# Kernel tuning notes

Measured on AMD Instinct MI355X. Metric: run time of the kernel, lower is better.

The kernel has to match this reference:

```python
import jax, jax.numpy as jnp
import numpy as np
import math

C = 256
GROUPS = 32
EPS = 1e-5

def setup_inputs() -> dict:
    key = jax.random.key(0)
    ks = jax.random.split(key, 11)
    B, H, W = 8, 64, 64
    s = 1.0 / math.sqrt(C)
    return {
        "x": jax.random.normal(ks[0], (B, C, H, W), dtype=jnp.float32),
        "gamma": jnp.ones((C,), jnp.float32),
        "beta": jnp.zeros((C,), jnp.float32),
        "wq": jax.random.normal(ks[1], (C, C), jnp.float32) * s,
        "bq": jnp.zeros((C,), jnp.float32),
        "wk": jax.random.normal(ks[2], (C, C), jnp.float32) * s,
        "bk": jnp.zeros((C,), jnp.float32),
        "wv": jax.random.normal(ks[3], (C, C), jnp.float32) * s,
        "bv": jnp.zeros((C,), jnp.float32),
        "wp": jax.random.normal(ks[4], (C, C), jnp.float32) * s,
        "bp": jnp.zeros((C,), jnp.float32),
    }

def _group_norm(x, gamma, beta):
    B, Cc, H, W = x.shape
    xg = x.reshape(B, GROUPS, Cc // GROUPS, H, W)
    mu = xg.mean(axis=(2, 3, 4), keepdims=True)
    var = xg.var(axis=(2, 3, 4), keepdims=True)
    xn = ((xg - mu) * jax.lax.rsqrt(var + EPS)).reshape(B, Cc, H, W)
    return xn * gamma[None, :, None, None] + beta[None, :, None, None]

def reference(x, gamma, beta, wq, bq, wk, bk, wv, bv, wp, bp):
    B, Cc, H, W = x.shape
    T = H * W
    h = _group_norm(x, gamma, beta)           # (B,C,H,W)
    hf = h.reshape(B, Cc, T)                  # (B,C,T)
    # 1x1 convs = per-pixel linear maps over channels
    q = jnp.einsum('oc,bct->bto', wq, hf) + bq           # (B,T,C)
    k = jnp.einsum('oc,bct->bot', wk, hf) + bk[:, None]  # (B,C,T)
    v = jnp.einsum('oc,bct->bto', wv, hf) + bv           # (B,T,C)
    scores = jnp.einsum('btc,bcs->bts', q, k) / math.sqrt(Cc)
    attn = jax.nn.softmax(scores, axis=-1)    # (B,T,T)
    z = jnp.einsum('bts,bsc->btc', attn, v)   # (B,T,C)
    zf = z.transpose(0, 2, 1)                 # (B,C,T)
    proj = jnp.einsum('oc,bct->bot', wp, zf) + bp[:, None]
    return x + proj.reshape(B, Cc, H, W)
```

## Files before the change

### kernel.cpp

```cpp
#include <hip/hip_runtime.h>


typedef unsigned short u16;
typedef unsigned char u8;
typedef __attribute__((ext_vector_type(8))) short short8;
typedef __attribute__((ext_vector_type(4))) float f32x4;

#define MFMA16(a, b, c) __builtin_amdgcn_mfma_f32_16x16x32_bf16((a), (b), (c), 0, 0, 0)
#define MFMA16F8(a, b, c) __builtin_amdgcn_mfma_f32_16x16x32_fp8_fp8((a), (b), (c), 0, 0, 0)

#define GLL16(g, l)                                                            \
  __builtin_amdgcn_global_load_lds(                                            \
      (const __attribute__((address_space(1))) void*)(g),                      \
      (__attribute__((address_space(3))) void*)(l), 16, 0, 0)

#define BAR_VM8()  asm volatile("s_waitcnt vmcnt(8)\n\ts_barrier" ::: "memory")
#define BAR_VM4()  asm volatile("s_waitcnt vmcnt(4)\n\ts_barrier" ::: "memory")
#define BAR_LGKM() asm volatile("s_waitcnt lgkmcnt(0)\n\ts_barrier" ::: "memory")

#define CVT_PK_BF16(dst, lo, hi)                                               \
  asm("v_cvt_pk_bf16_f32 %0, %1, %2" : "=v"(dst) : "v"(lo), "v"(hi))

__device__ __forceinline__ u16 f2bf(float f) {
  union { float f; unsigned u; } v; v.f = f;
  unsigned u = v.u;
  return (u16)((u + 0x7FFFu + ((u >> 16) & 1u)) >> 16);
}

__device__ __forceinline__ u8 f2fp8(float f) {
  int p = __builtin_amdgcn_cvt_pk_fp8_f32(f, f, 0, false);
  return (u8)(p & 0xff);
}

__global__ __launch_bounds__(256) void prep(
    const float* __restrict__ x,
    const float* __restrict__ gamma, const float* __restrict__ beta,
    const float* __restrict__ wq, const float* __restrict__ wk,
    const float* __restrict__ wv, const float* __restrict__ wp,
    u16* __restrict__ wb, u16* __restrict__ h_t) {
  const int bid = blockIdx.x, tid = threadIdx.x;
  if (bid < 256) {
    const int m = bid >> 6;
    const float* s = (m == 0) ? wq : (m == 1) ? wk : (m == 2) ? wv : wp;
    const int i = ((bid & 63) * 256 + tid) * 4;
    float4 v = *(const float4*)(s + i);
    u16* d = wb + m * 65536 + i;
    d[0] = f2bf(v.x); d[1] = f2bf(v.y); d[2] = f2bf(v.z); d[3] = f2bf(v.w);
    return;
  }
  const int gid = bid - 256;
  const int b = gid >> 5, g = gid & 31;
  const float* p = x + (long)gid * 32768;

  float s = 0.f, ss = 0.f;
  #pragma unroll 8
  for (int i = 0; i < 32; ++i) {
    float4 v = *(const float4*)(p + tid * 4 + i * 1024);
    s  += v.x + v.y + v.z + v.w;
    ss += v.x * v.x + v.y * v.y + v.z * v.z + v.w * v.w;
  }
  for (int off = 32; off; off >>= 1) {
    s  += __shfl_down(s, off);
    ss += __shfl_down(ss, off);
  }
  __shared__ float2 red[4];
  __shared__ float2 stat;
  if ((tid & 63) == 0) red[tid >> 6] = make_float2(s, ss);
  __syncthreads();
  if (tid == 0) {
    float S  = red[0].x + red[1].x + red[2].x + red[3].x;
    float SS = red[0].y + red[1].y + red[2].y + red[3].y;
    float mean = S * (1.f / 32768.f);
    float var  = SS * (1.f / 32768.f) - mean * mean;
    stat = make_float2(mean, rsqrtf(var + 1e-5f));
  }
  __syncthreads();
  const float mean = stat.x, rstd = stat.y;

  __shared__ float tile[8][257];
  const int cr = tid >> 5;
  const int c_g = g * 8;
  const float gm = gamma[c_g + cr] * rstd;
  const float bt = beta[c_g + cr] - mean * gm;
  const float* xc = x + ((long)(b * 256 + c_g + cr) * 4096);
  u16* hb = h_t + ((long)b * 4096) * 256 + c_g;

  for (int ch = 0; ch < 16; ++ch) {
    const int t0 = ch * 256;
    {
      const int tj = (tid & 31) * 8;
      float4 v0 = *(const float4*)(xc + t0 + tj);
      float4 v1 = *(const float4*)(xc + t0 + tj + 4);
      tile[cr][tj + 0] = v0.x * gm + bt;
      tile[cr][tj + 1] = v0.y * gm + bt;
      tile[cr][tj + 2] = v0.z * gm + bt;
      tile[cr][tj + 3] = v0.w * gm + bt;
      tile[cr][tj + 4] = v1.x * gm + bt;
      tile[cr][tj + 5] = v1.y * gm + bt;
      tile[cr][tj + 6] = v1.z * gm + bt;
      tile[cr][tj + 7] = v1.w * gm + bt;
    }
    __syncthreads();
    {
      uint4 o;
      CVT_PK_BF16(o.x, tile[0][tid], tile[1][tid]);
      CVT_PK_BF16(o.y, tile[2][tid], tile[3][tid]);
      CVT_PK_BF16(o.z, tile[4][tid], tile[5][tid]);
      CVT_PK_BF16(o.w, tile[6][tid], tile[7][tid]);
      *(uint4*)(hb + (long)(t0 + tid) * 256) = o;
    }
    __syncthreads();
  }
}

template <bool ROW_BIAS, bool RESID>
__global__ __launch_bounds__(256, 2) void gemm_bt(
    const u16* __restrict__ A, long strideAz, const u16* __restrict__ B,
    long strideBz, const float* __restrict__ bias, float scale,
    u16* __restrict__ outb, float* __restrict__ outf,
    const float* __restrict__ resid, long strideOz, int N) {
  __shared__ u16 a_lds[128 * 32];
  __shared__ u16 b_lds[128 * 32];
  const int tid = threadIdx.x, w = tid >> 6, l = tid & 63;
  const int l15 = l & 15, l4 = l >> 4;
  const int bz = blockIdx.z;
  A += bz * strideAz;
  B += bz * strideBz;
  const long obase = (long)bz * strideOz;
  const int m0 = blockIdx.y * 128, n0 = blockIdx.x * 128;
  const int wm = (w >> 1) * 64, wn = (w & 1) * 64;

  f32x4 acc[4][4];
  #pragma unroll
  for (int i = 0; i < 4; ++i)
    #pragma unroll
    for (int j = 0; j < 4; ++j) acc[i][j] = (f32x4)0.f;

  for (int kt = 0; kt < 8; ++kt) {
    const int k0 = kt * 32;
    __syncthreads();
    #pragma unroll
    for (int j = 0; j < 2; ++j) {
      const int r0 = (w * 2 + j) * 16;
      const int row = r0 + (l >> 2);
      const int sg = (l & 3) ^ (row & 3);
      GLL16(A + (long)(m0 + row) * 256 + k0 + sg * 8, a_lds + r0 * 32);
      GLL16(B + (long)(n0 + row) * 256 + k0 + sg * 8, b_lds + r0 * 32);
    }
    __syncthreads();
    short8 af[4], bf[4];
    #pragma unroll
    for (int t = 0; t < 4; ++t) {
      const int ra = wm + t * 16 + l15;
      af[t] = *(const short8*)(a_lds + ra * 32 + ((l4 ^ (ra & 3)) * 8));
      const int rb = wn + t * 16 + l15;
      bf[t] = *(const short8*)(b_lds + rb * 32 + ((l4 ^ (rb & 3)) * 8));
    }
    #pragma unroll
    for (int mt = 0; mt < 4; ++mt)
      #pragma unroll
      for (int nt = 0; nt < 4; ++nt) acc[mt][nt] = MFMA16(af[mt], bf[nt], acc[mt][nt]);
  }

  if (!ROW_BIAS) {
    float bv[4];
    #pragma unroll
    for (int nt = 0; nt < 4; ++nt) bv[nt] = bias[n0 + wn + nt * 16 + l15];
    #pragma unroll
    for (int mt = 0; mt < 4; ++mt)
      #pragma unroll
      for (int nt = 0; nt < 4; ++nt)
        #pragma unroll
        for (int r = 0; r < 4; ++r) {
          const int row = m0 + wm + mt * 16 + l4 * 4 + r;
          const int col = n0 + wn + nt * 16 + l15;
          outb[obase + (long)row * N + col] = f2bf((acc[mt][nt][r] + bv[nt]) * scale);
        }
  } else {
    float bm[4][4];
    #pragma unroll
    for (int mt = 0; mt < 4; ++mt)
      #pragma unroll
      for (int r = 0; r < 4; ++r) bm[mt][r] = bias[m0 + wm + mt * 16 + l4 * 4 + r];
    #pragma unroll
    for (int mt = 0; mt < 4; ++mt)
      #pragma unroll
      for (int nt = 0; nt < 4; ++nt)
        #pragma unroll
        for (int r = 0; r < 4; ++r) {
          const int row = m0 + wm + mt * 16 + l4 * 4 + r;
          const int col = n0 + wn + nt * 16 + l15;
          const long idx = obase + (long)row * N + col;
          float v = acc[mt][nt][r] + bm[mt][r];
          if (RESID) outf[idx] = v + resid[idx];
          else       outb[idx] = f2bf(v);
        }
  }
}

__global__ __launch_bounds__(256, 2) void gemm_qk(
    const u16* __restrict__ A, const u16* __restrict__ Bw,
    const float* __restrict__ bq, const float* __restrict__ bk,
    u8* __restrict__ Qs8, u8* __restrict__ Ks8) {
  __shared__ u16 a_lds[128 * 32];
  __shared__ u16 b_lds[128 * 32];
  const int tid = threadIdx.x, w = tid >> 6, l = tid & 63;
  const int l15 = l & 15, l4 = l >> 4;
  const int m0 = blockIdx.y * 128, n0 = blockIdx.x * 128;
  const int wm = (w >> 1) * 64, wn = (w & 1) * 64;

  f32x4 acc[4][4];
  #pragma unroll
  for (int i = 0; i < 4; ++i)
    #pragma unroll
    for (int j = 0; j < 4; ++j) acc[i][j] = (f32x4)0.f;

  for (int kt = 0; kt < 8; ++kt) {
    const int k0 = kt * 32;
    __syncthreads();
    #pragma unroll
    for (int j = 0; j < 2; ++j) {
      const int r0 = (w * 2 + j) * 16;
      const int row = r0 + (l >> 2);
      const int sg = (l & 3) ^ (row & 3);
      GLL16(A + (long)(m0 + row) * 256 + k0 + sg * 8, a_lds + r0 * 32);
      GLL16(Bw + (long)(n0 + row) * 256 + k0 + sg * 8, b_lds + r0 * 32);
    }
    __syncthreads();
    short8 af[4], bf[4];
    #pragma unroll
    for (int t = 0; t < 4; ++t) {
      const int ra = wm + t * 16 + l15;
      af[t] = *(const short8*)(a_lds + ra * 32 + ((l4 ^ (ra & 3)) * 8));
      const int rb = wn + t * 16 + l15;
      bf[t] = *(const short8*)(b_lds + rb * 32 + ((l4 ^ (rb & 3)) * 8));
    }
    #pragma unroll
    for (int mt = 0; mt < 4; ++mt)
      #pragma unroll
      for (int nt = 0; nt < 4; ++nt) acc[mt][nt] = MFMA16(af[mt], bf[nt], acc[mt][nt]);
  }

  const bool isQ = n0 < 256;
  u8* out = isQ ? Qs8 : Ks8;
  const float* bias = isQ ? bq : bk;
  const float osc = isQ ? 0.25f : 0.36067376022224085f;
  const int nc0 = n0 & 255;
  float bv[4];
  #pragma unroll
  for (int nt = 0; nt < 4; ++nt) bv[nt] = bias[nc0 + wn + nt * 16 + l15];
  #pragma unroll
  for (int mt = 0; mt < 4; ++mt)
    #pragma unroll
    for (int nt = 0; nt < 4; ++nt)
      #pragma unroll
      for (int r = 0; r < 4; ++r) {
        const int row = m0 + wm + mt * 16 + l4 * 4 + r;
        const int col = nc0 + wn + nt * 16 + l15;
        out[(long)row * 256 + col] = f2fp8((acc[mt][nt][r] + bv[nt]) * osc);
      }
}

__global__ __launch_bounds__(256, 2) void attn_kernel(
    const u8* __restrict__ Qs8, const u8* __restrict__ Ks8,
    const u16* __restrict__ Vt, u16* __restrict__ Z) {
  __shared__ u8  k_lds8[16384];
  __shared__ u16 v_lds[16384];
  __shared__ u16 p_lds[64 * 72];
  __shared__ float l_red[256];

  const int tid = threadIdx.x, w = tid >> 6, l = tid & 63;
  const int l15 = l & 15, l4 = l >> 4;
  const int bid = blockIdx.x;
  const int batch = bid & 7;
  const int qt = bid >> 3;
  const int ws0 = (w & 1) * 32, wq0 = (w >> 1) * 32, wcolO = (w & 1) * 128;
  const long qrow_base = (long)batch * 4096 + qt * 64;

  const u8*  kbase = Ks8 + (long)batch * 4096 * 256;
  const u16* vbase = Vt + (long)batch * 256 * 4096;

  long qf[2][8];
  {
    const u8* qp = Qs8 + (qrow_base + wq0) * 256;
    #pragma unroll
    for (int qt2 = 0; qt2 < 2; ++qt2)
      #pragma unroll
      for (int ks = 0; ks < 8; ++ks)
        qf[qt2][ks] = *(const long*)(qp + (qt2 * 16 + l15) * 256 + ks * 32 + l4 * 8);
  }

  const int cvv = 8 * w + (l >> 3);
  const int sgv = (l & 7) ^ (cvv & 7);

  f32x4 o_acc[2][8];
  #pragma unroll
  for (int mt = 0; mt < 2; ++mt)
    #pragma unroll
    for (int nt = 0; nt < 8; ++nt) o_acc[mt][nt] = (f32x4)0.f;
  float rs2[2] = {0.f, 0.f};

  #pragma unroll
  for (int j = 0; j < 4; ++j) {
    const int r0 = (j * 4 + w) * 4;
    const int row = r0 + (l >> 4);
    const int g = (l & 15) ^ (row & 15);
    GLL16(kbase + (long)row * 256 + g * 16, k_lds8 + r0 * 256);
  }
  #pragma unroll
  for (int j = 0; j < 8; ++j) {
    const int c0 = (j * 4 + w) * 8;
    GLL16(vbase + (long)(c0 + (l >> 3)) * 4096 + sgv * 8, v_lds + c0 * 64);
  }

  for (int st = 0; st < 64; ++st) {
    const int snn = ((st + 1) & 63) * 64;

    BAR_VM8();

    f32x4 sacc[2][2];
    #pragma unroll
    for (int i = 0; i < 2; ++i)
      #pragma unroll
      for (int j = 0; j < 2; ++j) sacc[i][j] = (f32x4)0.f;
    __builtin_amdgcn_s_setprio(1);
    #pragma unroll
    for (int ks = 0; ks < 8; ++ks) {
      long kf[2];
      #pragma unroll
      for (int st2 = 0; st2 < 2; ++st2) {
        const int row = ws0 + st2 * 16 + l15;
        const int g = (ks * 2 + (l4 >> 1)) ^ l15;
        kf[st2] = *(const long*)(k_lds8 + row * 256 + g * 16 + (l4 & 1) * 8);
      }
      #pragma unroll
      for (int st2 = 0; st2 < 2; ++st2)
        #pragma unroll
        for (int qt2 = 0; qt2 < 2; ++qt2)
          sacc[st2][qt2] = MFMA16F8(kf[st2], qf[qt2][ks], sacc[st2][qt2]);
    }
    __builtin_amdgcn_s_setprio(0);

    #pragma unroll
    for (int st2 = 0; st2 < 2; ++st2)
      #pragma unroll
      for (int qt2 = 0; qt2 < 2; ++qt2) {
        float e0 = __builtin_exp2f(sacc[st2][qt2][0]);
        float e1 = __builtin_exp2f(sacc[st2][qt2][1]);
        float e2 = __builtin_exp2f(sacc[st2][qt2][2]);
        float e3 = __builtin_exp2f(sacc[st2][qt2][3]);
        rs2[qt2] += (e0 + e1) + (e2 + e3);
        unsigned pw0, pw1;
        CVT_PK_BF16(pw0, e0, e1);
        CVT_PK_BF16(pw1, e2, e3);
        *(uint2*)(p_lds + (wq0 + qt2 * 16 + l15) * 72 + ws0 + st2 * 16 + l4 * 4) =
            make_uint2(pw0, pw1);
      }

    BAR_LGKM();

    #pragma unroll
    for (int j = 0; j < 4; ++j) {
      const int r0 = (j * 4 + w) * 4;
      const int row = r0 + (l >> 4);
      const int g = (l & 15) ^ (row & 15);
      GLL16(kbase + (long)(snn + row) * 256 + g * 16, k_lds8 + r0 * 256);
    }

    BAR_VM4();

    __builtin_amdgcn_s_setprio(1);
    #pragma unroll
    for (int ks2 = 0; ks2 < 2; ++ks2) {
      short8 pa[2];
      #pragma unroll
      for (int mt = 0; mt < 2; ++mt)
        pa[mt] = *(const short8*)(p_lds + (wq0 + mt * 16 + l15) * 72 + ks2 * 32 + l4 * 8);
      #pragma unroll
      for (int nt = 0; nt < 8; ++nt) {
        const int c = wcolO + nt * 16 + l15;
        const int gv = (ks2 * 4 + l4) ^ (c & 7);
        short8 vb = *(const short8*)(v_lds + c * 64 + gv * 8);
        #pragma unroll
        for (int mt = 0; mt < 2; ++mt) o_acc[mt][nt] = MFMA16(pa[mt], vb, o_acc[mt][nt]);
      }
    }
    __builtin_amdgcn_s_setprio(0);

    BAR_LGKM();

    #pragma unroll
    for (int j = 0; j < 8; ++j) {
      const int c0 = (j * 4 + w) * 8;
      GLL16(vbase + (long)(c0 + (l >> 3)) * 4096 + snn + sgv * 8, v_lds + c0 * 64);
    }
  }

  #pragma unroll
  for (int qt2 = 0; qt2 < 2; ++qt2) {
    float v = rs2[qt2];
    v += __shfl_xor(v, 16);
    v += __shfl_xor(v, 32);
    if (l4 == 0) l_red[w * 64 + wq0 + qt2 * 16 + l15] = v;
  }
  __syncthreads();
  if (tid < 64) {
    const int w0 = (tid >> 5) * 2;
    float t = l_red[w0 * 64 + tid] + l_red[(w0 + 1) * 64 + tid];
    l_red[tid] = 1.f / t;
  }
  __syncthreads();

  #pragma unroll
  for (int mt = 0; mt < 2; ++mt) {
    float inv[4];
    #pragma unroll
    for (int r = 0; r < 4; ++r) inv[r] = l_red[wq0 + mt * 16 + l4 * 4 + r];
    #pragma unroll
    for (int nt = 0; nt < 8; ++nt) {
      const int col = wcolO + nt * 16 + l15;
      #pragma unroll
      for (int r = 0; r < 4; ++r) {
        const long row = qrow_base + wq0 + mt * 16 + l4 * 4 + r;
        Z[row * 256 + col] = f2bf(o_acc[mt][nt][r] * inv[r]);
      }
    }
  }
}

extern "C" void kernel_launch(void* const* d_in, const int* in_sizes, int n_in,
                              void* d_out, int out_size, void* d_ws, size_t ws_size,
                              hipStream_t stream) {
  (void)in_sizes; (void)n_in; (void)out_size; (void)ws_size;
  const float* x     = (const float*)d_in[0];
  const float* gamma = (const float*)d_in[1];
  const float* beta  = (const float*)d_in[2];
  const float* wq    = (const float*)d_in[3];
  const float* bq    = (const float*)d_in[4];
  const float* wk    = (const float*)d_in[5];
  const float* bk    = (const float*)d_in[6];
  const float* wv    = (const float*)d_in[7];
  const float* bv    = (const float*)d_in[8];
  const float* wp    = (const float*)d_in[9];
  const float* bp    = (const float*)d_in[10];
  float* out = (float*)d_out;

  char* ws = (char*)d_ws;
  u16*    wb    = (u16*)(ws);
  u16*    h_t   = (u16*)(ws + 526336);
  u8*     Qs8   = (u8*)(ws + 17303552);
  u8*     Ks8   = (u8*)(ws + 25692160);
  u16*    Vt    = (u16*)(ws + 34080768);
  u16*    Zb    = (u16*)(ws + 50857984);

  prep<<<dim3(512), dim3(256), 0, stream>>>(x, gamma, beta, wq, wk, wv, wp,
                                            wb, h_t);

  const long sB = 4096L * 256L, sO = 256L * 4096L;
  gemm_qk<<<dim3(4, 256), dim3(256), 0, stream>>>(h_t, wb, bq, bk, Qs8, Ks8);
  gemm_bt<true, false><<<dim3(32, 2, 8), dim3(256), 0, stream>>>(
      wb + 2 * 65536, 0L, h_t, sB, bv, 1.0f, Vt, nullptr, nullptr, sO, 4096);

  attn_kernel<<<dim3(512), dim3(256), 0, stream>>>(Qs8, Ks8, Vt, Zb);

  gemm_bt<true, true><<<dim3(32, 2, 8), dim3(256), 0, stream>>>(
      wb + 3 * 65536, 0L, Zb, sB, bp, 1.0f, nullptr, out, x, sO, 4096);
}
```

Measured before the change: 297.7 us.

## Switch attention kernel MFMAs from 16x16 to 32x32 tiles

Replaces the 16x16x32 fp8 and bf16 MFMA instructions in the attention kernel with 32x32x16 variants. QK^T now uses one 32x32 tile per wave, split into two interleaved accumulators that are summed before exp. The PV stage is re-partitioned so each wave owns 64 output columns across all 64 query rows. The aim is fewer LDS fragment reads per FLOP and fewer MFMA issues. In exchange it changes the LDS access patterns and register layout, and the larger-tile instructions have longer latency.

```diff
diff --git a/kernel.cpp b/kernel.cpp
--- a/kernel.cpp
+++ b/kernel.cpp
@@ -5,9 +5,11 @@
 typedef unsigned char u8;
 typedef __attribute__((ext_vector_type(8))) short short8;
 typedef __attribute__((ext_vector_type(4))) float f32x4;
+typedef __attribute__((ext_vector_type(16))) float f32x16;
 
 #define MFMA16(a, b, c) __builtin_amdgcn_mfma_f32_16x16x32_bf16((a), (b), (c), 0, 0, 0)
-#define MFMA16F8(a, b, c) __builtin_amdgcn_mfma_f32_16x16x32_fp8_fp8((a), (b), (c), 0, 0, 0)
+#define MFMA32(a, b, c) __builtin_amdgcn_mfma_f32_32x32x16_bf16((a), (b), (c), 0, 0, 0)
+#define MFMA32F8(a, b, c) __builtin_amdgcn_mfma_f32_32x32x16_fp8_fp8((a), (b), (c), 0, 0, 0)
 
 #define GLL16(g, l)                                                            \
   __builtin_amdgcn_global_load_lds(                                            \
@@ -271,34 +273,33 @@
 
   const int tid = threadIdx.x, w = tid >> 6, l = tid & 63;
   const int l15 = l & 15, l4 = l >> 4;
+  const int l31 = l & 31, lh = l >> 5;
   const int bid = blockIdx.x;
   const int batch = bid & 7;
   const int qt = bid >> 3;
-  const int ws0 = (w & 1) * 32, wq0 = (w >> 1) * 32, wcolO = (w & 1) * 128;
+  const int ws0 = (w & 1) * 32, wq0 = (w >> 1) * 32;
+  const int wcolO = w * 64;
   const long qrow_base = (long)batch * 4096 + qt * 64;
 
   const u8*  kbase = Ks8 + (long)batch * 4096 * 256;
   const u16* vbase = Vt + (long)batch * 256 * 4096;
 
-  long qf[2][8];
+  long qf[16];
   {
-    const u8* qp = Qs8 + (qrow_base + wq0) * 256;
-    #pragma unroll
-    for (int qt2 = 0; qt2 < 2; ++qt2)
-      #pragma unroll
-      for (int ks = 0; ks < 8; ++ks)
-        qf[qt2][ks] = *(const long*)(qp + (qt2 * 16 + l15) * 256 + ks * 32 + l4 * 8);
+    const u8* qp = Qs8 + (qrow_base + wq0 + l31) * 256 + lh * 8;
+    #pragma unroll
+    for (int st = 0; st < 16; ++st) qf[st] = *(const long*)(qp + st * 16);
   }
 
   const int cvv = 8 * w + (l >> 3);
   const int sgv = (l & 7) ^ (cvv & 7);
 
-  f32x4 o_acc[2][8];
+  f32x16 o_acc[2][2];
   #pragma unroll
   for (int mt = 0; mt < 2; ++mt)
     #pragma unroll
-    for (int nt = 0; nt < 8; ++nt) o_acc[mt][nt] = (f32x4)0.f;
-  float rs2[2] = {0.f, 0.f};
+    for (int nt = 0; nt < 2; ++nt) o_acc[mt][nt] = (f32x16)0.f;
+  float rs = 0.f;
 
   #pragma unroll
   for (int j = 0; j < 4; ++j) {
@@ -318,44 +319,29 @@
 
     BAR_VM8();
 
-    f32x4 sacc[2][2];
-    #pragma unroll
-    for (int i = 0; i < 2; ++i)
-      #pragma unroll
-      for (int j = 0; j < 2; ++j) sacc[i][j] = (f32x4)0.f;
+    f32x16 sa = (f32x16)0.f, sb = (f32x16)0.f;
     __builtin_amdgcn_s_setprio(1);
     #pragma unroll
-    for (int ks = 0; ks < 8; ++ks) {
-      long kf[2];
-      #pragma unroll
-      for (int st2 = 0; st2 < 2; ++st2) {
-        const int row = ws0 + st2 * 16 + l15;
-        const int g = (ks * 2 + (l4 >> 1)) ^ l15;
-        kf[st2] = *(const long*)(k_lds8 + row * 256 + g * 16 + (l4 & 1) * 8);
-      }
-      #pragma unroll
-      for (int st2 = 0; st2 < 2; ++st2)
-        #pragma unroll
-        for (int qt2 = 0; qt2 < 2; ++qt2)
-          sacc[st2][qt2] = MFMA16F8(kf[st2], qf[qt2][ks], sacc[st2][qt2]);
+    for (int ks = 0; ks < 16; ++ks) {
+      long kf = *(const long*)(k_lds8 + (ws0 + l31) * 256 + (ks ^ l15) * 16 + lh * 8);
+      if (ks & 1) sb = MFMA32F8(kf, qf[ks], sb);
+      else        sa = MFMA32F8(kf, qf[ks], sa);
     }
     __builtin_amdgcn_s_setprio(0);
 
     #pragma unroll
-    for (int st2 = 0; st2 < 2; ++st2)
-      #pragma unroll
-      for (int qt2 = 0; qt2 < 2; ++qt2) {
-        float e0 = __builtin_exp2f(sacc[st2][qt2][0]);
-        float e1 = __builtin_exp2f(sacc[st2][qt2][1]);
-        float e2 = __builtin_exp2f(sacc[st2][qt2][2]);
-        float e3 = __builtin_exp2f(sacc[st2][qt2][3]);
-        rs2[qt2] += (e0 + e1) + (e2 + e3);
-        unsigned pw0, pw1;
-        CVT_PK_BF16(pw0, e0, e1);
-        CVT_PK_BF16(pw1, e2, e3);
-        *(uint2*)(p_lds + (wq0 + qt2 * 16 + l15) * 72 + ws0 + st2 * 16 + l4 * 4) =
-            make_uint2(pw0, pw1);
-      }
+    for (int t = 0; t < 4; ++t) {
+      float e0 = __builtin_exp2f(sa[4 * t + 0] + sb[4 * t + 0]);
+      float e1 = __builtin_exp2f(sa[4 * t + 1] + sb[4 * t + 1]);
+      float e2 = __builtin_exp2f(sa[4 * t + 2] + sb[4 * t + 2]);
+      float e3 = __builtin_exp2f(sa[4 * t + 3] + sb[4 * t + 3]);
+      rs += (e0 + e1) + (e2 + e3);
+      unsigned pw0, pw1;
+      CVT_PK_BF16(pw0, e0, e1);
+      CVT_PK_BF16(pw1, e2, e3);
+      *(uint2*)(p_lds + (wq0 + l31) * 72 + ws0 + 8 * t + 4 * lh) =
+          make_uint2(pw0, pw1);
+    }
 
     BAR_LGKM();
 
@@ -371,18 +357,18 @@
 
     __builtin_amdgcn_s_setprio(1);
     #pragma unroll
-    for (int ks2 = 0; ks2 < 2; ++ks2) {
+    for (int ks2 = 0; ks2 < 4; ++ks2) {
       short8 pa[2];
       #pragma unroll
       for (int mt = 0; mt < 2; ++mt)
-        pa[mt] = *(const short8*)(p_lds + (wq0 + mt * 16 + l15) * 72 + ks2 * 32 + l4 * 8);
-      #pragma unroll
-      for (int nt = 0; nt < 8; ++nt) {
-        const int c = wcolO + nt * 16 + l15;
-        const int gv = (ks2 * 4 + l4) ^ (c & 7);
+        pa[mt] = *(const short8*)(p_lds + (mt * 32 + l31) * 72 + ks2 * 16 + lh * 8);
+      #pragma unroll
+      for (int nt = 0; nt < 2; ++nt) {
+        const int c = wcolO + nt * 32 + l31;
+        const int gv = (ks2 * 2 + lh) ^ (c & 7);
         short8 vb = *(const short8*)(v_lds + c * 64 + gv * 8);
         #pragma unroll
-        for (int mt = 0; mt < 2; ++mt) o_acc[mt][nt] = MFMA16(pa[mt], vb, o_acc[mt][nt]);
+        for (int mt = 0; mt < 2; ++mt) o_acc[mt][nt] = MFMA32(pa[mt], vb, o_acc[mt][nt]);
       }
     }
     __builtin_amdgcn_s_setprio(0);
@@ -396,12 +382,10 @@
     }
   }
 
-  #pragma unroll
-  for (int qt2 = 0; qt2 < 2; ++qt2) {
-    float v = rs2[qt2];
-    v += __shfl_xor(v, 16);
+  {
+    float v = rs;
     v += __shfl_xor(v, 32);
-    if (l4 == 0) l_red[w * 64 + wq0 + qt2 * 16 + l15] = v;
+    if (lh == 0) l_red[w * 64 + wq0 + l31] = v;
   }
   __syncthreads();
   if (tid < 64) {
@@ -413,16 +397,20 @@
 
   #pragma unroll
   for (int mt = 0; mt < 2; ++mt) {
-    float inv[4];
-    #pragma unroll
-    for (int r = 0; r < 4; ++r) inv[r] = l_red[wq0 + mt * 16 + l4 * 4 + r];
-    #pragma unroll
-    for (int nt = 0; nt < 8; ++nt) {
-      const int col = wcolO + nt * 16 + l15;
-      #pragma unroll
-      for (int r = 0; r < 4; ++r) {
-        const long row = qrow_base + wq0 + mt * 16 + l4 * 4 + r;
-        Z[row * 256 + col] = f2bf(o_acc[mt][nt][r] * inv[r]);
+    #pragma unroll
+    for (int t = 0; t < 4; ++t) {
+      float inv[4];
+      #pragma unroll
+      for (int r2 = 0; r2 < 4; ++r2)
+        inv[r2] = l_red[mt * 32 + 8 * t + 4 * lh + r2];
+      #pragma unroll
+      for (int nt = 0; nt < 2; ++nt) {
+        const int col = wcolO + nt * 32 + l31;
+        #pragma unroll
+        for (int r2 = 0; r2 < 4; ++r2) {
+          const long row = qrow_base + mt * 32 + 8 * t + 4 * lh + r2;
+          Z[row * 256 + col] = f2bf(o_acc[mt][nt][4 * t + r2] * inv[r2]);
+        }
       }
     }
   }
```

After: 295.8 us. About the same (-0.6%).
